# Kernel optimization log

Hardware: AMD Instinct MI355X
Metric: run time of the kernel (lower is better)

Reference implementation:

```python
import jax, jax.numpy as jnp
import numpy as np

NUM_HEADS = 12
LATENT = 768
HEAD_DIM = LATENT // NUM_HEADS
SCALE = float(np.sqrt(LATENT))  # note: sqrt(latent_vector_size), not sqrt(head_dim), per source


def setup_inputs() -> dict:
    key = jax.random.key(0)
    ks = jax.random.split(key, 7)
    B, S, D = 8, 1024, LATENT
    std = 1.0 / np.sqrt(D)
    return {
        "x": jax.random.normal(ks[0], (B, S, D), dtype=jnp.float32),
        "Wq": jax.random.normal(ks[1], (D, D), dtype=jnp.float32) * std,
        "bq": jnp.zeros((D,), dtype=jnp.float32),
        "Wk": jax.random.normal(ks[2], (D, D), dtype=jnp.float32) * std,
        "bk": jnp.zeros((D,), dtype=jnp.float32),
        "Wv": jax.random.normal(ks[3], (D, D), dtype=jnp.float32) * std,
        "bv": jnp.zeros((D,), dtype=jnp.float32),
    }


def reference(x, Wq, bq, Wk, bk, Wv, bv):
    B, S, D = x.shape
    H, Hd = NUM_HEADS, HEAD_DIM
    # torch Linear: y = x @ W.T + b
    q = (x @ Wq.T + bq).reshape(B, S, H, Hd).transpose(0, 2, 1, 3)  # [B,H,S,Hd]
    k = (x @ Wk.T + bk).reshape(B, S, H, Hd).transpose(0, 2, 1, 3)
    v = (x @ Wv.T + bv).reshape(B, S, H, Hd).transpose(0, 2, 1, 3)
    qk = jnp.einsum("bhsd,bhtd->bhst", q, k) / SCALE  # [B,H,S,S]
    A = jax.nn.softmax(qk, axis=-1)
    # dropout(0.1) treated as eval-mode identity
    out = jnp.einsum("bhst,bhtd->bhsd", A, v)  # [B,H,S,Hd]
    out = out.transpose(0, 2, 1, 3).reshape(B, S, D)
    return (out, A)
```

## Files before the change

### kernel.cpp

```cpp
#include <hip/hip_runtime.h>
#include <stdint.h>

typedef __bf16 bf16_t;
typedef __bf16 bf16x4 __attribute__((ext_vector_type(4)));
typedef __bf16 bf16x8 __attribute__((ext_vector_type(8)));
typedef float f32x4 __attribute__((ext_vector_type(4)));

#define MFMA(a, b, c) __builtin_amdgcn_mfma_f32_16x16x32_bf16(a, b, c, 0, 0, 0)

typedef __attribute__((address_space(3))) uint32_t as3_u32;
typedef __attribute__((address_space(1))) uint32_t as1_u32;
__device__ __forceinline__ void gload_lds16(const void* g, void* l) {
  __builtin_amdgcn_global_load_lds((as1_u32*)g, (as3_u32*)l, 16, 0, 0);
}

__global__ void cvt_all(const float* __restrict__ x, const float* __restrict__ wq,
                        const float* __restrict__ wk, const float* __restrict__ wv,
                        bf16_t* __restrict__ dst) {
  int i = blockIdx.x * blockDim.x + threadIdx.x;
  if (i >= 2015232) return;
  const float* src; int off;
  if (i < 1572864) { src = x; off = i; }
  else {
    int j = i - 1572864;
    if (j < 147456)      { src = wq; off = j; }
    else if (j < 294912) { src = wk; off = j - 147456; }
    else                 { src = wv; off = j - 294912; }
  }
  const f32x4 v = reinterpret_cast<const f32x4*>(src)[off];
  bf16x4 o = { (bf16_t)v.x, (bf16_t)v.y, (bf16_t)v.z, (bf16_t)v.w };
  reinterpret_cast<bf16x4*>(dst)[i] = o;
}

__global__ __launch_bounds__(256)
void qkv_gemm(const bf16_t* __restrict__ X, const bf16_t* __restrict__ Wb,
              const float* __restrict__ bq, const float* __restrict__ bk,
              const float* __restrict__ bv,
              bf16_t* __restrict__ Qo, bf16_t* __restrict__ Ko, bf16_t* __restrict__ Vo)
{
  __shared__ __align__(16) bf16_t smem[17408];
  bf16_t* const sA0 = smem;
  bf16_t* const sA1 = smem + 4096;
  bf16_t* const sB0 = smem + 8192;
  bf16_t* const sB1 = smem + 12288;
  bf16_t* const ep  = smem;

  const int tid = threadIdx.x;
  const int lane = tid & 63, w = tid >> 6;
  const int wr = w >> 1, wc = w & 1;
  const int lq = lane & 15, lg = lane >> 4;
  const int m0 = blockIdx.x * 128;
  const int n0 = blockIdx.y * 128;
  const int z  = blockIdx.z;

  const bf16_t* W = Wb + z * 589824;
  const float* bias = (z == 0) ? bq : (z == 1) ? bk : bv;

  const int arow = wr * 64, brow = wc * 64;
  const int sr = tid >> 2, scc = (tid & 3) * 8;

  const bf16_t* gA = X + (m0 + sr) * 768 + scc;
  const bf16_t* gB = W + (n0 + sr) * 768 + scc;
  const int ko = lg * 8;

  f32x4 acc[4][4] = {};

#define STAGE(bufA, bufB, kt)                                            \
  do {                                                                   \
    const int kk_ = (kt) * 32;                                           \
    gload_lds16(gA + kk_,             &bufA[tid * 8]);                   \
    gload_lds16(gA + kk_ + 64 * 768,  &bufA[(tid + 256) * 8]);           \
    gload_lds16(gB + kk_,             &bufB[tid * 8]);                   \
    gload_lds16(gB + kk_ + 64 * 768,  &bufB[(tid + 256) * 8]);           \
  } while (0)

#define COMPUTE(bufA, bufB)                                              \
  do {                                                                   \
    bf16x8 af[4], bfr[4];                                                \
    _Pragma("unroll")                                                    \
    for (int mf = 0; mf < 4; ++mf)                                       \
      af[mf] = *(const bf16x8*)&bufA[(arow + mf * 16 + lq) * 32 + ko];   \
    _Pragma("unroll")                                                    \
    for (int nf = 0; nf < 4; ++nf)                                       \
      bfr[nf] = *(const bf16x8*)&bufB[(brow + nf * 16 + lq) * 32 + ko];  \
    _Pragma("unroll")                                                    \
    for (int mf = 0; mf < 4; ++mf)                                       \
      _Pragma("unroll")                                                  \
      for (int nf = 0; nf < 4; ++nf)                                     \
        acc[mf][nf] = MFMA(af[mf], bfr[nf], acc[mf][nf]);                \
  } while (0)

  STAGE(sA0, sB0, 0);
  for (int kt = 0; kt < 24; kt += 2) {
    __syncthreads();
    STAGE(sA1, sB1, kt + 1);
    COMPUTE(sA0, sB0);
    __syncthreads();
    if (kt + 2 < 24) STAGE(sA0, sB0, kt + 2);
    COMPUTE(sA1, sB1);
  }
  __syncthreads();

  const int b = m0 >> 10, sq0 = m0 & 1023;

  if (z < 2) {
#pragma unroll
    for (int nf = 0; nf < 4; ++nf) {
      const int c = brow + nf * 16 + lq;
      const float bval = bias[n0 + c];
#pragma unroll
      for (int mf = 0; mf < 4; ++mf)
#pragma unroll
        for (int jr = 0; jr < 4; ++jr)
          ep[(arow + mf * 16 + lg * 4 + jr) * 136 + c] = (bf16_t)(acc[mf][nf][jr] + bval);
    }
    __syncthreads();
    bf16_t* dst = (z == 0) ? Qo : Ko;
#pragma unroll
    for (int nh = 0; nh < 2; ++nh) {
      const int h = (n0 >> 6) + nh;
#pragma unroll
      for (int rp = 0; rp < 2; ++rp) {
        const int r = (tid >> 2) + rp * 64;
        bf16_t* o = dst + ((size_t)(b * 12 + h) * 1024 + sq0 + r) * 64;
        const bf16_t* s = &ep[r * 136 + nh * 64];
#pragma unroll
        for (int i = 0; i < 2; ++i) {
          const int ch = (tid & 3) + i * 4;
          *(bf16x8*)(o + ch * 8) = *(const bf16x8*)(s + ch * 8);
        }
      }
    }
  } else {
#pragma unroll
    for (int nf = 0; nf < 4; ++nf) {
      const int c = brow + nf * 16 + lq;
      const float bval = bias[n0 + c];
#pragma unroll
      for (int mf = 0; mf < 4; ++mf) {
        const int r0 = arow + mf * 16 + lg * 4;
        bf16x4 pv = { (bf16_t)(acc[mf][nf][0] + bval), (bf16_t)(acc[mf][nf][1] + bval),
                      (bf16_t)(acc[mf][nf][2] + bval), (bf16_t)(acc[mf][nf][3] + bval) };
        *(bf16x4*)&ep[c * 136 + r0] = pv;
      }
    }
    __syncthreads();
    const int c = tid >> 1;
    const int h = (n0 >> 6) + (c >> 6), dd = c & 63;
    bf16_t* o = Vo + ((size_t)(b * 12 + h) * 64 + dd) * 1024 + sq0;
    const bf16_t* s = &ep[c * 136];
#pragma unroll
    for (int i = 0; i < 8; ++i) {
      const int ch = (tid & 1) + i * 2;
      *(bf16x8*)(o + ch * 8) = *(const bf16x8*)(s + ch * 8);
    }
  }
#undef STAGE
#undef COMPUTE
}

__global__ __launch_bounds__(256)
void attn_kernel(const bf16_t* __restrict__ Q, const bf16_t* __restrict__ K,
                 const bf16_t* __restrict__ V, float* __restrict__ out,
                 float* __restrict__ Aout)
{
  __shared__ __align__(16) bf16_t Pl[32 * 1032];
  __shared__ __align__(16) bf16_t Ql[32 * 72];
  __shared__ float red[4][32];
  __shared__ float inv_s[32];

  const int tid = threadIdx.x, lane = tid & 63, w = tid >> 6;
  const int lq = lane & 15, lg = lane >> 4;
  const int bh = blockIdx.x, q0 = blockIdx.y * 32;

  const bf16_t* Qp = Q + (bh * 1024 + q0) * 64;
  const bf16_t* Kp = K + bh * 1024 * 64;
  const bf16_t* Vt = V + bh * 64 * 1024;

  {
    const int q = tid >> 3, du = (tid & 7) * 8;
    *(bf16x8*)&Ql[q * 72 + du] = *(const bf16x8*)(Qp + q * 64 + du);
  }
  __syncthreads();

  const float CEXP = 1.4426950408889634f / 27.712812921102035f;

  bf16x8 bqf[2][2];
#pragma unroll
  for (int dh = 0; dh < 2; ++dh)
#pragma unroll
    for (int qf = 0; qf < 2; ++qf)
      bqf[dh][qf] = *(const bf16x8*)&Ql[(qf * 16 + lq) * 72 + dh * 32 + lg * 8];

  float psum0 = 0.f, psum1 = 0.f;

  for (int i = 0; i < 4; ++i) {
    const int t0 = (w + i * 4) * 64;
    bf16x8 af[4][2];
#pragma unroll
    for (int mf = 0; mf < 4; ++mf) {
      const bf16_t* kp = Kp + (t0 + mf * 16 + lq) * 64 + lg * 8;
      af[mf][0] = *(const bf16x8*)(kp);
      af[mf][1] = *(const bf16x8*)(kp + 32);
    }
#pragma unroll
    for (int mf = 0; mf < 4; ++mf) {
#pragma unroll
      for (int qf = 0; qf < 2; ++qf) {
        f32x4 acc = {};
        acc = MFMA(af[mf][0], bqf[0][qf], acc);
        acc = MFMA(af[mf][1], bqf[1][qf], acc);
        float p0 = exp2f(acc[0] * CEXP);
        float p1 = exp2f(acc[1] * CEXP);
        float p2 = exp2f(acc[2] * CEXP);
        float p3 = exp2f(acc[3] * CEXP);
        if (qf == 0) psum0 += p0 + p1 + p2 + p3;
        else         psum1 += p0 + p1 + p2 + p3;
        bf16x4 pv = { (bf16_t)p0, (bf16_t)p1, (bf16_t)p2, (bf16_t)p3 };
        const int q = qf * 16 + lq;
        const int tt = t0 + mf * 16 + lg * 4;
        *(bf16x4*)&Pl[q * 1032 + tt] = pv;
      }
    }
  }

  psum0 += __shfl_xor(psum0, 16); psum0 += __shfl_xor(psum0, 32);
  psum1 += __shfl_xor(psum1, 16); psum1 += __shfl_xor(psum1, 32);
  if (lane < 16) { red[w][lane] = psum0; red[w][16 + lane] = psum1; }
  __syncthreads();
  if (tid < 32)
    inv_s[tid] = 1.0f / (red[0][tid] + red[1][tid] + red[2][tid] + red[3][tid]);
  __syncthreads();

  const int r8 = 8 * w;
  float* const Ap0 = Aout + ((size_t)bh * 1024 + q0) * 1024;

  f32x4 oacc[2] = {};
  for (int ks = 0; ks < 32; ++ks) {
    const int kc = ks * 32;
    bf16x8 vb = *(const bf16x8*)(Vt + (w * 16 + lq) * 1024 + kc + lg * 8);
#pragma unroll
    for (int mf = 0; mf < 2; ++mf) {
      bf16x8 pa = *(const bf16x8*)&Pl[(mf * 16 + lq) * 1032 + kc + lg * 8];
      oacc[mf] = MFMA(pa, vb, oacc[mf]);
    }
    const int ar = r8 + (ks & 7);
    const int cc = (ks >> 3) * 256;
    const float ainv = inv_s[ar];
    bf16x4 pv = *(const bf16x4*)&Pl[ar * 1032 + cc + lane * 4];
    f32x4 o = { (float)pv[0] * ainv, (float)pv[1] * ainv,
                (float)pv[2] * ainv, (float)pv[3] * ainv };
    __builtin_nontemporal_store(o, (f32x4*)(Ap0 + (size_t)ar * 1024 + cc + lane * 4));
  }

  __syncthreads();
  float* const Ol = (float*)Pl;
#pragma unroll
  for (int mf = 0; mf < 2; ++mf)
#pragma unroll
    for (int jr = 0; jr < 4; ++jr) {
      const int q = mf * 16 + lg * 4 + jr;
      Ol[q * 68 + w * 16 + lq] = oacc[mf][jr] * inv_s[q];
    }
  __syncthreads();
  {
    const int b = bh / 12, h = bh % 12;
    const int r = tid >> 3, cchunk = (tid & 7) * 8;
    float* op = out + ((size_t)b * 1024 + q0 + r) * 768 + h * 64 + cchunk;
    f32x4 o0 = *(const f32x4*)&Ol[r * 68 + cchunk];
    f32x4 o1 = *(const f32x4*)&Ol[r * 68 + cchunk + 4];
    *(f32x4*)(op)     = o0;
    *(f32x4*)(op + 4) = o1;
  }
}

extern "C" void kernel_launch(void* const* d_in, const int* in_sizes, int n_in,
                              void* d_out, int out_size, void* d_ws, size_t ws_size,
                              hipStream_t stream) {
  (void)in_sizes; (void)n_in; (void)out_size; (void)ws_size;
  const float* x  = (const float*)d_in[0];
  const float* Wq = (const float*)d_in[1];
  const float* bq = (const float*)d_in[2];
  const float* Wk = (const float*)d_in[3];
  const float* bk = (const float*)d_in[4];
  const float* Wv = (const float*)d_in[5];
  const float* bv = (const float*)d_in[6];

  float* out  = (float*)d_out;
  float* Aout = out + 6291456;

  bf16_t* ws   = (bf16_t*)d_ws;
  bf16_t* x_bf = ws;
  bf16_t* w_bf = ws + 6291456;
  bf16_t* q_ws = ws + 8060928;
  bf16_t* k_ws = ws + 14352384;
  bf16_t* v_ws = ws + 20643840;

  cvt_all<<<7872, 256, 0, stream>>>(x, Wq, Wk, Wv, ws);
  qkv_gemm<<<dim3(64, 6, 3), 256, 0, stream>>>(x_bf, w_bf, bq, bk, bv, q_ws, k_ws, v_ws);
  attn_kernel<<<dim3(96, 32), 256, 0, stream>>>(q_ws, k_ws, v_ws, out, Aout);
}
```

Measured before the change: 173.8 us.

## Recompute QK scores in a second pass instead of storing full P row in LDS

The attention kernel no longer keeps a 32x1024 bf16 probability tile in shared memory (~66KB). The first pass now only accumulates softmax row sums. A second pass recomputes QK^T per 128-column chunk into a double-buffered 2x32x136 LDS tile, applies the normalisation before the bf16 cast, writes A, and runs the PV MFMAs. This cuts LDS use, allowing more blocks per CU, at the cost of doubling the QK MFMAs and exp work plus a barrier per chunk.

New measurement: 207.1 us. +19.1%, slower.

```diff
diff --git a/kernel.cpp b/kernel.cpp
--- a/kernel.cpp
+++ b/kernel.cpp
@@ -164,8 +164,8 @@
                  const bf16_t* __restrict__ V, float* __restrict__ out,
                  float* __restrict__ Aout)
 {
-  __shared__ __align__(16) bf16_t Pl[32 * 1032];
   __shared__ __align__(16) bf16_t Ql[32 * 72];
+  __shared__ __align__(16) bf16_t Pc[2][32 * 136];
   __shared__ float red[4][32];
   __shared__ float inv_s[32];
 
@@ -193,7 +193,6 @@
       bqf[dh][qf] = *(const bf16x8*)&Ql[(qf * 16 + lq) * 72 + dh * 32 + lg * 8];
 
   float psum0 = 0.f, psum1 = 0.f;
-
   for (int i = 0; i < 4; ++i) {
     const int t0 = (w + i * 4) * 64;
     bf16x8 af[4][2];
@@ -210,16 +209,9 @@
         f32x4 acc = {};
         acc = MFMA(af[mf][0], bqf[0][qf], acc);
         acc = MFMA(af[mf][1], bqf[1][qf], acc);
-        float p0 = exp2f(acc[0] * CEXP);
-        float p1 = exp2f(acc[1] * CEXP);
-        float p2 = exp2f(acc[2] * CEXP);
-        float p3 = exp2f(acc[3] * CEXP);
-        if (qf == 0) psum0 += p0 + p1 + p2 + p3;
-        else         psum1 += p0 + p1 + p2 + p3;
-        bf16x4 pv = { (bf16_t)p0, (bf16_t)p1, (bf16_t)p2, (bf16_t)p3 };
-        const int q = qf * 16 + lq;
-        const int tt = t0 + mf * 16 + lg * 4;
-        *(bf16x4*)&Pl[q * 1032 + tt] = pv;
+        float s = exp2f(acc[0] * CEXP) + exp2f(acc[1] * CEXP)
+                + exp2f(acc[2] * CEXP) + exp2f(acc[3] * CEXP);
+        if (qf == 0) psum0 += s; else psum1 += s;
       }
     }
   }
@@ -232,35 +224,68 @@
     inv_s[tid] = 1.0f / (red[0][tid] + red[1][tid] + red[2][tid] + red[3][tid]);
   __syncthreads();
 
-  const int r8 = 8 * w;
-  float* const Ap0 = Aout + ((size_t)bh * 1024 + q0) * 1024;
-
+  const float inv0 = inv_s[lq];
+  const float inv1 = inv_s[16 + lq];
+
+  const int ar = tid >> 3, ac = tid & 7;
+  float* const ApR = Aout + ((size_t)bh * 1024 + q0 + ar) * 1024;
   f32x4 oacc[2] = {};
-  for (int ks = 0; ks < 32; ++ks) {
-    const int kc = ks * 32;
-    bf16x8 vb = *(const bf16x8*)(Vt + (w * 16 + lq) * 1024 + kc + lg * 8);
+
+  for (int c = 0; c < 8; ++c) {
+    bf16_t* const buf = Pc[c & 1];
+    const int tsub = c * 128 + w * 32;
+
 #pragma unroll
     for (int mf = 0; mf < 2; ++mf) {
-      bf16x8 pa = *(const bf16x8*)&Pl[(mf * 16 + lq) * 1032 + kc + lg * 8];
-      oacc[mf] = MFMA(pa, vb, oacc[mf]);
-    }
-    const int ar = r8 + (ks & 7);
-    const int cc = (ks >> 3) * 256;
-    const float ainv = inv_s[ar];
-    bf16x4 pv = *(const bf16x4*)&Pl[ar * 1032 + cc + lane * 4];
-    f32x4 o = { (float)pv[0] * ainv, (float)pv[1] * ainv,
-                (float)pv[2] * ainv, (float)pv[3] * ainv };
-    __builtin_nontemporal_store(o, (f32x4*)(Ap0 + (size_t)ar * 1024 + cc + lane * 4));
-  }
-
-  __syncthreads();
-  float* const Ol = (float*)Pl;
+      const bf16_t* kp = Kp + (tsub + mf * 16 + lq) * 64 + lg * 8;
+      bf16x8 a0 = *(const bf16x8*)(kp);
+      bf16x8 a1 = *(const bf16x8*)(kp + 32);
+#pragma unroll
+      for (int qf = 0; qf < 2; ++qf) {
+        f32x4 acc = {};
+        acc = MFMA(a0, bqf[0][qf], acc);
+        acc = MFMA(a1, bqf[1][qf], acc);
+        const float inv = (qf == 0) ? inv0 : inv1;
+        bf16x4 pv = { (bf16_t)(exp2f(acc[0] * CEXP) * inv),
+                      (bf16_t)(exp2f(acc[1] * CEXP) * inv),
+                      (bf16_t)(exp2f(acc[2] * CEXP) * inv),
+                      (bf16_t)(exp2f(acc[3] * CEXP) * inv) };
+        *(bf16x4*)&buf[(qf * 16 + lq) * 136 + w * 32 + mf * 16 + lg * 4] = pv;
+      }
+    }
+    __syncthreads();
+
+    {
+      float* const Ap = ApR + c * 128;
+      const bf16_t* const ps = &buf[ar * 136];
+#pragma unroll
+      for (int j = 0; j < 4; ++j) {
+        const int col = ac * 4 + j * 32;
+        bf16x4 pv = *(const bf16x4*)(ps + col);
+        f32x4 o = { (float)pv[0], (float)pv[1], (float)pv[2], (float)pv[3] };
+        __builtin_nontemporal_store(o, (f32x4*)(Ap + col));
+      }
+    }
+
+#pragma unroll
+    for (int ks = 0; ks < 4; ++ks) {
+      bf16x8 vb = *(const bf16x8*)(Vt + (w * 16 + lq) * 1024 + c * 128 + ks * 32 + lg * 8);
+#pragma unroll
+      for (int mf = 0; mf < 2; ++mf) {
+        bf16x8 pa = *(const bf16x8*)&buf[(mf * 16 + lq) * 136 + ks * 32 + lg * 8];
+        oacc[mf] = MFMA(pa, vb, oacc[mf]);
+      }
+    }
+  }
+
+  __syncthreads();
+  float* const Ol = (float*)Pc;
 #pragma unroll
   for (int mf = 0; mf < 2; ++mf)
 #pragma unroll
     for (int jr = 0; jr < 4; ++jr) {
       const int q = mf * 16 + lg * 4 + jr;
-      Ol[q * 68 + w * 16 + lq] = oacc[mf][jr] * inv_s[q];
+      Ol[q * 68 + w * 16 + lq] = oacc[mf][jr];
     }
   __syncthreads();
   {
```

## Double attention block to 512 threads with split-K PV reduction

Applied to the files above, without the earlier changes.

Moves the attention kernel from four to eight waves per block. The QK/exp phase now gives each wave fewer key tiles, and the PV phase splits the key dimension across two wave groups whose partial outputs are summed through LDS. The aim is more latency hiding and more parallelism per 32-query tile, at the cost of an extra LDS reduction and possibly lower occupancy from the larger blocks.

After: 170.4 us. 1.02x faster.

```diff
diff --git a/kernel.cpp b/kernel.cpp
--- a/kernel.cpp
+++ b/kernel.cpp
@@ -159,14 +159,14 @@
 #undef COMPUTE
 }
 
-__global__ __launch_bounds__(256)
+__global__ __launch_bounds__(512)
 void attn_kernel(const bf16_t* __restrict__ Q, const bf16_t* __restrict__ K,
                  const bf16_t* __restrict__ V, float* __restrict__ out,
                  float* __restrict__ Aout)
 {
   __shared__ __align__(16) bf16_t Pl[32 * 1032];
   __shared__ __align__(16) bf16_t Ql[32 * 72];
-  __shared__ float red[4][32];
+  __shared__ float red[8][32];
   __shared__ float inv_s[32];
 
   const int tid = threadIdx.x, lane = tid & 63, w = tid >> 6;
@@ -177,7 +177,7 @@
   const bf16_t* Kp = K + bh * 1024 * 64;
   const bf16_t* Vt = V + bh * 64 * 1024;
 
-  {
+  if (tid < 256) {
     const int q = tid >> 3, du = (tid & 7) * 8;
     *(bf16x8*)&Ql[q * 72 + du] = *(const bf16x8*)(Qp + q * 64 + du);
   }
@@ -194,8 +194,8 @@
 
   float psum0 = 0.f, psum1 = 0.f;
 
-  for (int i = 0; i < 4; ++i) {
-    const int t0 = (w + i * 4) * 64;
+  for (int i = 0; i < 2; ++i) {
+    const int t0 = (w + i * 8) * 64;
     bf16x8 af[4][2];
 #pragma unroll
     for (int mf = 0; mf < 4; ++mf) {
@@ -228,24 +228,29 @@
   psum1 += __shfl_xor(psum1, 16); psum1 += __shfl_xor(psum1, 32);
   if (lane < 16) { red[w][lane] = psum0; red[w][16 + lane] = psum1; }
   __syncthreads();
-  if (tid < 32)
-    inv_s[tid] = 1.0f / (red[0][tid] + red[1][tid] + red[2][tid] + red[3][tid]);
-  __syncthreads();
-
-  const int r8 = 8 * w;
+  if (tid < 32) {
+    float s = 0.f;
+#pragma unroll
+    for (int j = 0; j < 8; ++j) s += red[j][tid];
+    inv_s[tid] = 1.0f / s;
+  }
+  __syncthreads();
+
+  const int dq = w & 3, kh = w >> 2;
+  const int r4 = 4 * w;
   float* const Ap0 = Aout + ((size_t)bh * 1024 + q0) * 1024;
 
   f32x4 oacc[2] = {};
-  for (int ks = 0; ks < 32; ++ks) {
-    const int kc = ks * 32;
-    bf16x8 vb = *(const bf16x8*)(Vt + (w * 16 + lq) * 1024 + kc + lg * 8);
+  for (int ks = 0; ks < 16; ++ks) {
+    const int kc = (kh * 16 + ks) * 32;
+    bf16x8 vb = *(const bf16x8*)(Vt + (dq * 16 + lq) * 1024 + kc + lg * 8);
 #pragma unroll
     for (int mf = 0; mf < 2; ++mf) {
       bf16x8 pa = *(const bf16x8*)&Pl[(mf * 16 + lq) * 1032 + kc + lg * 8];
       oacc[mf] = MFMA(pa, vb, oacc[mf]);
     }
-    const int ar = r8 + (ks & 7);
-    const int cc = (ks >> 3) * 256;
+    const int ar = r4 + (ks & 3);
+    const int cc = (ks >> 2) * 256;
     const float ainv = inv_s[ar];
     bf16x4 pv = *(const bf16x4*)&Pl[ar * 1032 + cc + lane * 4];
     f32x4 o = { (float)pv[0] * ainv, (float)pv[1] * ainv,
@@ -260,17 +265,18 @@
 #pragma unroll
     for (int jr = 0; jr < 4; ++jr) {
       const int q = mf * 16 + lg * 4 + jr;
-      Ol[q * 68 + w * 16 + lq] = oacc[mf][jr] * inv_s[q];
+      Ol[kh * 2176 + q * 68 + dq * 16 + lq] = oacc[mf][jr];
     }
   __syncthreads();
   {
     const int b = bh / 12, h = bh % 12;
-    const int r = tid >> 3, cchunk = (tid & 7) * 8;
-    float* op = out + ((size_t)b * 1024 + q0 + r) * 768 + h * 64 + cchunk;
-    f32x4 o0 = *(const f32x4*)&Ol[r * 68 + cchunk];
-    f32x4 o1 = *(const f32x4*)&Ol[r * 68 + cchunk + 4];
-    *(f32x4*)(op)     = o0;
-    *(f32x4*)(op + 4) = o1;
+    const int r = tid >> 4, c4 = (tid & 15) * 4;
+    const float s = inv_s[r];
+    f32x4 p0 = *(const f32x4*)&Ol[r * 68 + c4];
+    f32x4 p1 = *(const f32x4*)&Ol[2176 + r * 68 + c4];
+    f32x4 o = { (p0[0] + p1[0]) * s, (p0[1] + p1[1]) * s,
+                (p0[2] + p1[2]) * s, (p0[3] + p1[3]) * s };
+    *(f32x4*)(out + ((size_t)b * 1024 + q0 + r) * 768 + h * 64 + c4) = o;
   }
 }
 
@@ -298,5 +304,5 @@
 
   cvt_all<<<7872, 256, 0, stream>>>(x, Wq, Wk, Wv, ws);
   qkv_gemm<<<dim3(64, 6, 3), 256, 0, stream>>>(x_bf, w_bf, bq, bk, bv, q_ws, k_ws, v_ws);
-  attn_kernel<<<dim3(96, 32), 256, 0, stream>>>(q_ws, k_ws, v_ws, out, Aout);
-}
+  attn_kernel<<<dim3(96, 32), 512, 0, stream>>>(q_ws, k_ws, v_ws, out, Aout);
+}
```
